# Optimization experiments

Hardware: AMD Instinct MI355X
Metric: run time of the kernel (lower is better)

Reference implementation:

```python
import jax, jax.numpy as jnp
import numpy as np

REG = 1e-6

def maxpool2(x):  # NCHW, kernel 2 stride 2
    return jax.lax.reduce_window(x, -jnp.inf, jax.lax.max, (1, 1, 2, 2), (1, 1, 2, 2), 'VALID')

def conv2d_same(x, w, b):  # NCHW / OIHW, stride 1, padding 1 (3x3)
    y = jax.lax.conv_general_dilated(x, w, (1, 1), ((1, 1), (1, 1)),
                                     dimension_numbers=('NCHW', 'OIHW', 'NCHW'))
    return y + b[None, :, None, None]

def batch_skew(a):  # [B,3] -> [B,3,3]
    z = jnp.zeros_like(a[:, 0])
    return jnp.stack([
        jnp.stack([z, -a[:, 2], a[:, 1]], -1),
        jnp.stack([a[:, 2], z, -a[:, 0]], -1),
        jnp.stack([-a[:, 1], a[:, 0], z], -1)], 1)

def batch_twist2mat(w):  # Rodrigues: so(3) -> SO(3)
    theta = jnp.maximum(jnp.linalg.norm(w, axis=1, keepdims=True), 1e-12)  # [B,1]
    A = batch_skew(w / theta)
    s = jnp.sin(theta)[:, :, None]
    c = (1.0 - jnp.cos(theta))[:, :, None]
    return jnp.eye(3, dtype=w.dtype) + s * A + c * (A @ A)

def setup_inputs() -> dict:
    key = jax.random.key(0)
    ks = jax.random.split(key, 24)
    B, C, H, W = 64, 8, 240, 320
    HW = H * W
    A = jax.random.normal(ks[0], (B, 6, 6), jnp.float32)
    JtJ = A @ jnp.swapaxes(A, 1, 2) + 6.0 * jnp.eye(6, dtype=jnp.float32)  # SPD Hessian
    inp = {
        'JtJ': JtJ,
        'Jt': jax.random.normal(ks[1], (B, 6, HW), jnp.float32),
        'weights': jax.random.uniform(ks[2], (B, 1, H, W), jnp.float32),
        'R': jax.random.normal(ks[3], (B, 1, H, W), jnp.float32),
        'pose_R': jax.random.normal(ks[4], (B, 3, 3), jnp.float32),
        'pose_t': jax.random.normal(ks[5], (B, 3, 1), jnp.float32),
        'invD0': jax.random.uniform(ks[6], (B, 1, H, W), jnp.float32),
        'invD1': jax.random.uniform(ks[7], (B, 1, H, W), jnp.float32),
        'x0': jax.random.normal(ks[8], (B, C, H, W), jnp.float32),
        'x1': jax.random.normal(ks[9], (B, C, H, W), jnp.float32),
        'K': jax.random.normal(ks[10], (B, 3, 3), jnp.float32),
        # DampingNet parameters
        'consts': jax.random.normal(ks[11], (6, 6), jnp.float32),
        'conv1_w': jax.random.normal(ks[12], (8, 1, 3, 3), jnp.float32) * 0.2,
        'conv1_b': jnp.zeros((8,), jnp.float32),
        'conv2_w': jax.random.normal(ks[13], (16, 8, 3, 3), jnp.float32) * 0.1,
        'conv2_b': jnp.zeros((16,), jnp.float32),
        'fc1_w': jax.random.normal(ks[14], (64, 19200), jnp.float32) * 0.01,
        'fc1_b': jnp.zeros((64,), jnp.float32),
        'fc2_w': jax.random.normal(ks[15], (6, 64), jnp.float32) * 0.1,
        'fc2_b': jnp.zeros((6,), jnp.float32),
    }
    return inp

def dampingnet(R, consts, c1w, c1b, c2w, c2b, f1w, f1b, f2w, f2b):
    B = R.shape[0]
    h = maxpool2(R)
    h = jax.nn.relu(conv2d_same(h, c1w, c1b))
    h = maxpool2(h)
    h = jax.nn.relu(conv2d_same(h, c2w, c2b))
    h = maxpool2(h)
    h = h.reshape(B, -1)  # [B, 19200], NCHW flatten matches torch
    h = jax.nn.relu(h @ f1w.T + f1b)
    lambdas_w = jax.nn.softmax(h @ f2w.T + f2b, axis=-1)  # [B,6]
    wc = lambdas_w @ consts  # [B,6]
    min_, max_ = -6.0, -5.0
    return 10.0 ** (min_ + jax.nn.sigmoid(wc) * (max_ - min_))  # [B,6]

def reference(JtJ, Jt, weights, R, pose_R, pose_t, invD0, invD1, x0, x1, K,
              consts, conv1_w, conv1_b, conv2_w, conv2_b, fc1_w, fc1_b, fc2_w, fc2_b):
    B = JtJ.shape[0]
    wR = (weights * R).reshape(B, -1, 1)            # [B,HW,1]
    JtR = Jt @ wR                                   # [B,6,1]
    lam = dampingnet(R, consts, conv1_w, conv1_b, conv2_w, conv2_b,
                     fc1_w, fc1_b, fc2_w, fc2_b)    # [B,6]
    trace = jnp.trace(JtJ, axis1=1, axis2=2)        # [B]
    diag_add = lam + 1e-6 * trace[:, None]          # [B,6]
    eye6 = jnp.eye(6, dtype=JtJ.dtype)
    Hessian = JtJ + diag_add[:, :, None] * eye6     # diag_mask*lambda + epsilon
    # inverse_update_pose: regularized batched 6x6 inverse
    Hinv = jnp.linalg.inv(Hessian + REG * eye6)
    xi = Hinv @ JtR                                 # [B,6,1]
    d_R = batch_twist2mat(-xi[:, :3, 0])            # [B,3,3]
    d_t = -(d_R @ xi[:, 3:])                        # [B,3,1]
    R_new = pose_R @ d_R
    t_new = pose_R @ d_t + pose_t
    return jnp.concatenate([R_new, t_new], axis=2)  # [B,3,4] pose (R|t)
```

## Files before the change

kernel.cpp:

```cpp
#include <hip/hip_runtime.h>
#include <math.h>

#define BATCH 64
#define WW 320
#define HWTOT 76800
#define HW4 19200
#define NJTRB 512
#define JSL4 2400
#define NCONV1 1280
#define KS 96
#define NSLICE 200

__global__ __launch_bounds__(256) void k_front(
    const float* __restrict__ Jt, const float* __restrict__ wgt,
    const float* __restrict__ Rin, const float* __restrict__ c1w,
    const float* __restrict__ c1b, float* __restrict__ part,
    float* __restrict__ h1) {
  __shared__ float smem[34 * 37 + 96];
  int tid = threadIdx.x;
  if (blockIdx.x < NJTRB) {
    int b = blockIdx.x >> 3, s = blockIdx.x & 7;
    const float4* w4 = (const float4*)(wgt + (size_t)b * HWTOT);
    const float4* r4 = (const float4*)(Rin + (size_t)b * HWTOT);
    const float4* j4 = (const float4*)(Jt + (size_t)b * 6 * HWTOT);
    int base = s * JSL4;
    float acc[6] = {0.f, 0.f, 0.f, 0.f, 0.f, 0.f};
#pragma unroll 3
    for (int k = 0; k < 9; ++k) {
      int t = base + k * 256 + tid;
      float4 wv = w4[t], rv = r4[t];
      float4 p;
      p.x = wv.x * rv.x; p.y = wv.y * rv.y; p.z = wv.z * rv.z; p.w = wv.w * rv.w;
#pragma unroll
      for (int i = 0; i < 6; ++i) {
        float4 jv = j4[i * HW4 + t];
        acc[i] += jv.x * p.x + jv.y * p.y + jv.z * p.z + jv.w * p.w;
      }
    }
    if (tid < 96) {
      int t = base + 2304 + tid;
      float4 wv = w4[t], rv = r4[t];
      float4 p;
      p.x = wv.x * rv.x; p.y = wv.y * rv.y; p.z = wv.z * rv.z; p.w = wv.w * rv.w;
#pragma unroll
      for (int i = 0; i < 6; ++i) {
        float4 jv = j4[i * HW4 + t];
        acc[i] += jv.x * p.x + jv.y * p.y + jv.z * p.z + jv.w * p.w;
      }
    }
#pragma unroll
    for (int i = 0; i < 6; ++i) {
      float v = acc[i];
      for (int off = 32; off; off >>= 1) v += __shfl_down(v, off, 64);
      acc[i] = v;
    }
    float* sred = smem;
    int lane = tid & 63, wid = tid >> 6;
    if (lane == 0) {
#pragma unroll
      for (int i = 0; i < 6; ++i) sred[wid * 6 + i] = acc[i];
    }
    __syncthreads();
    if (tid < 6) {
      part[blockIdx.x * 6 + tid] =
          sred[0 + tid] + sred[6 + tid] + sred[12 + tid] + sred[18 + tid];
    }
    return;
  }
  int cb = blockIdx.x - NJTRB;
  int b = cb / 20, rem = cb % 20;
  int by = rem / 5, bx = rem % 5;
  float (*sA)[37] = (float(*)[37])smem;
  float* sW = smem + 34 * 37;
  float* sB = sW + 72;
  if (tid < 72) sW[tid] = c1w[(tid & 7) * 9 + (tid >> 3)];
  if (tid < 8) sB[tid] = c1b[tid];
  int iy0 = 32 * by - 1;
  const float* src = Rin + (size_t)b * HWTOT;
  for (int idx = tid; idx < 34 * 18; idx += 256) {
    int pr = idx / 18, c4 = idx % 18;
    int py = iy0 + pr;
    int gx = 64 * bx - 4 + 4 * c4;
    float cell0 = 0.f, cell1 = 0.f;
    if (py >= 0 && py < 120 && gx >= 0 && gx < 320) {
      const float4* row0 = (const float4*)(src + (size_t)(2 * py) * WW + gx);
      const float4* row1 = (const float4*)(src + (size_t)(2 * py + 1) * WW + gx);
      float4 v0 = row0[0], v1 = row1[0];
      cell0 = fmaxf(fmaxf(v0.x, v0.y), fmaxf(v1.x, v1.y));
      cell1 = fmaxf(fmaxf(v0.z, v0.w), fmaxf(v1.z, v1.w));
    }
    sA[pr][2 * c4] = cell0;
    sA[pr][2 * c4 + 1] = cell1;
  }
  __syncthreads();
  int ly = tid / 16, lx = tid % 16;
  int y = 16 * by + ly, x = 16 * bx + lx;
  float win[16];
#pragma unroll
  for (int r = 0; r < 4; ++r)
#pragma unroll
    for (int c = 0; c < 4; ++c) win[r * 4 + c] = sA[2 * ly + r][2 * lx + c + 1];
  float acc[8][4];
#pragma unroll
  for (int oc = 0; oc < 8; ++oc)
#pragma unroll
    for (int p = 0; p < 4; ++p) acc[oc][p] = 0.f;
#pragma unroll
  for (int tap = 0; tap < 9; ++tap) {
    int ky = tap / 3, kx = tap % 3;
#pragma unroll
    for (int oc = 0; oc < 8; ++oc) {
      float wv = sW[tap * 8 + oc];
#pragma unroll
      for (int py = 0; py < 2; ++py)
#pragma unroll
        for (int px = 0; px < 2; ++px)
          acc[oc][py * 2 + px] += wv * win[(py + ky) * 4 + (px + kx)];
    }
  }
  if (y < 60) {
    float v[8];
#pragma unroll
    for (int oc = 0; oc < 8; ++oc)
      v[oc] = fmaxf(fmaxf(fmaxf(acc[oc][0], acc[oc][1]), fmaxf(acc[oc][2], acc[oc][3])) + sB[oc], 0.f);
    float4* dst = (float4*)(h1 + (((size_t)b * 60 + y) * 80 + x) * 8);
    dst[0] = make_float4(v[0], v[1], v[2], v[3]);
    dst[1] = make_float4(v[4], v[5], v[6], v[7]);
  }
}

__global__ __launch_bounds__(256) void k_conv2(
    const float* __restrict__ h1, const float* __restrict__ c2w,
    const float* __restrict__ c2b, float* __restrict__ h2) {
  __shared__ float sA[8][34][37];
  __shared__ __align__(16) float sW[576];
  __shared__ float sB[8];
  int b = blockIdx.z >> 1, ocg = blockIdx.z & 1;
  int ty0 = blockIdx.y * 16, tx0 = blockIdx.x * 16;
  int tid = threadIdx.x;
  for (int i = tid; i < 576; i += 256) {
    int ic = i / 72, tap = (i % 72) / 8, o = i % 8;
    sW[i] = c2w[(ocg * 8 + o) * 72 + ic * 9 + tap];
  }
  if (tid < 8) sB[tid] = c2b[ocg * 8 + tid];
  int iy0 = ty0 * 2 - 1, ix0 = tx0 * 2 - 1;
  const float* src = h1 + (size_t)b * 60 * 80 * 8;
  for (int idx = tid; idx < 34 * 34; idx += 256) {
    int r = idx / 34, c = idx % 34;
    int gy = iy0 + r, gx = ix0 + c;
    float4 v0 = make_float4(0.f, 0.f, 0.f, 0.f), v1 = v0;
    if (gy >= 0 && gy < 60 && gx >= 0 && gx < 80) {
      const float4* p = (const float4*)(src + ((size_t)gy * 80 + gx) * 8);
      v0 = p[0]; v1 = p[1];
    }
    sA[0][r][c] = v0.x; sA[1][r][c] = v0.y; sA[2][r][c] = v0.z; sA[3][r][c] = v0.w;
    sA[4][r][c] = v1.x; sA[5][r][c] = v1.y; sA[6][r][c] = v1.z; sA[7][r][c] = v1.w;
  }
  __syncthreads();
  int ly = tid / 16, lx = tid % 16;
  int y = ty0 + ly, x = tx0 + lx;
  float acc[8][4];
#pragma unroll
  for (int oc = 0; oc < 8; ++oc)
#pragma unroll
    for (int p = 0; p < 4; ++p) acc[oc][p] = 0.f;
  const float4* sW4 = (const float4*)sW;
#pragma unroll 1
  for (int ic = 0; ic < 8; ++ic) {
    float win[16];
#pragma unroll
    for (int r = 0; r < 4; ++r)
#pragma unroll
      for (int c = 0; c < 4; ++c) win[r * 4 + c] = sA[ic][2 * ly + r][2 * lx + c];
#pragma unroll
    for (int tap = 0; tap < 9; ++tap) {
      int ky = tap / 3, kx = tap % 3;
#pragma unroll
      for (int q = 0; q < 2; ++q) {
        float4 w4v = sW4[(ic * 9 + tap) * 2 + q];
        float warr[4] = {w4v.x, w4v.y, w4v.z, w4v.w};
#pragma unroll
        for (int c4 = 0; c4 < 4; ++c4) {
          float wv = warr[c4];
          int oc = q * 4 + c4;
#pragma unroll
          for (int py = 0; py < 2; ++py)
#pragma unroll
            for (int px = 0; px < 2; ++px)
              acc[oc][py * 2 + px] += wv * win[(py + ky) * 4 + (px + kx)];
        }
      }
    }
  }
  if (y < 30 && x < 40) {
#pragma unroll
    for (int o = 0; o < 8; ++o) {
      int oc = ocg * 8 + o;
      float m = fmaxf(fmaxf(acc[o][0], acc[o][1]), fmaxf(acc[o][2], acc[o][3])) + sB[o];
      h2[(((size_t)b * 16 + oc) * 30 + y) * 40 + x] = fmaxf(m, 0.f);
    }
  }
}

__global__ __launch_bounds__(256) void k_fc1_part(
    const float* __restrict__ h2, const float* __restrict__ f1w,
    float* __restrict__ fcpart) {
  __shared__ __align__(16) float sH[KS * 68];
  __shared__ __align__(16) float sWt[KS * 68];
  int sl = blockIdx.x, k0 = sl * KS;
  int tid = threadIdx.x;
  for (int idx = tid; idx < 64 * KS; idx += 256) {
    int b = idx / KS, kk = idx % KS;
    sH[kk * 68 + b] = h2[(size_t)b * 19200 + k0 + kk];
    sWt[kk * 68 + b] = f1w[(size_t)b * 19200 + k0 + kk];
  }
  __syncthreads();
  int bq = tid & 15, jq = tid >> 4;
  int b0 = bq * 4, j0 = jq * 4;
  float acc[4][4];
#pragma unroll
  for (int i = 0; i < 4; ++i)
#pragma unroll
    for (int j = 0; j < 4; ++j) acc[i][j] = 0.f;
  for (int kk = 0; kk < KS; ++kk) {
    float4 hv = *(const float4*)&sH[kk * 68 + b0];
    float4 wv = *(const float4*)&sWt[kk * 68 + j0];
    float hb[4] = {hv.x, hv.y, hv.z, hv.w};
    float wb[4] = {wv.x, wv.y, wv.z, wv.w};
#pragma unroll
    for (int i = 0; i < 4; ++i)
#pragma unroll
      for (int j = 0; j < 4; ++j) acc[i][j] += hb[i] * wb[j];
  }
#pragma unroll
  for (int i = 0; i < 4; ++i)
#pragma unroll
    for (int j = 0; j < 4; ++j)
      fcpart[(size_t)sl * 4096 + (b0 + i) * 64 + (j0 + j)] = acc[i][j];
}

__global__ __launch_bounds__(256) void k_final(
    const float* __restrict__ fcpart, const float* __restrict__ f1b,
    const float* __restrict__ f2w, const float* __restrict__ f2b,
    const float* __restrict__ consts, const float* __restrict__ part,
    const float* __restrict__ JtJ, const float* __restrict__ poseR,
    const float* __restrict__ poseT, float* __restrict__ out) {
  __shared__ float sfc[4][64];
  __shared__ float fc1v[64];
  __shared__ float lg[6];
  __shared__ float lamv[6];
  __shared__ float jtrv[6];
  int b = blockIdx.x, tid = threadIdx.x;
  int g = tid >> 6, j = tid & 63;
  float a = 0.f;
  for (int s = g; s < NSLICE; s += 4) a += fcpart[(size_t)s * 4096 + b * 64 + j];
  sfc[g][j] = a;
  __syncthreads();
  if (tid < 64)
    fc1v[tid] = fmaxf(sfc[0][tid] + sfc[1][tid] + sfc[2][tid] + sfc[3][tid] + f1b[tid], 0.f);
  if (tid >= 64 && tid < 70) {
    int i = tid - 64;
    float v = 0.f;
    for (int s = 0; s < 8; ++s) v += part[(b * 8 + s) * 6 + i];
    jtrv[i] = v;
  }
  __syncthreads();
  if (tid < 6) {
    float v = f2b[tid];
#pragma unroll
    for (int k = 0; k < 64; ++k) v += fc1v[k] * f2w[tid * 64 + k];
    lg[tid] = v;
  }
  __syncthreads();
  if (tid < 6) {
    float m = lg[0];
#pragma unroll
    for (int i = 1; i < 6; ++i) m = fmaxf(m, lg[i]);
    float e[6], ssum = 0.f;
#pragma unroll
    for (int i = 0; i < 6; ++i) { e[i] = expf(lg[i] - m); ssum += e[i]; }
    float inv = 1.f / ssum;
    float wc = 0.f;
#pragma unroll
    for (int i = 0; i < 6; ++i) wc += (e[i] * inv) * consts[i * 6 + tid];
    float sg = 1.f / (1.f + expf(-wc));
    lamv[tid] = expf((-6.f + sg) * 2.302585092994046f);
  }
  __syncthreads();
  if (tid == 0) {
    float Hm[6][6];
    const float* srcH = JtJ + b * 36;
    float tr = 0.f;
#pragma unroll
    for (int i = 0; i < 6; ++i) {
#pragma unroll
      for (int jj = 0; jj < 6; ++jj) Hm[i][jj] = srcH[i * 6 + jj];
      tr += srcH[i * 6 + i];
    }
    float rhs[6];
#pragma unroll
    for (int i = 0; i < 6; ++i) {
      rhs[i] = jtrv[i];
      Hm[i][i] += lamv[i] + 1e-6f * tr + 1e-6f;
    }
    float L[6][6];
#pragma unroll
    for (int i = 0; i < 6; ++i) {
#pragma unroll
      for (int jj = 0; jj < 6; ++jj) {
        if (jj > i) continue;
        float s = Hm[i][jj];
#pragma unroll
        for (int k = 0; k < 6; ++k)
          if (k < jj) s -= L[i][k] * L[jj][k];
        if (i == jj) L[i][jj] = sqrtf(fmaxf(s, 1e-30f));
        else L[i][jj] = s / L[jj][jj];
      }
    }
    float yv[6];
#pragma unroll
    for (int i = 0; i < 6; ++i) {
      float s = rhs[i];
#pragma unroll
      for (int k = 0; k < 6; ++k)
        if (k < i) s -= L[i][k] * yv[k];
      yv[i] = s / L[i][i];
    }
    float xi[6];
#pragma unroll
    for (int ii = 5; ii >= 0; --ii) {
      float s = yv[ii];
#pragma unroll
      for (int k = 0; k < 6; ++k)
        if (k > ii) s -= L[k][ii] * xi[k];
      xi[ii] = s / L[ii][ii];
    }
    float wx = -xi[0], wy = -xi[1], wz = -xi[2];
    float th = fmaxf(sqrtf(wx * wx + wy * wy + wz * wz), 1e-12f);
    float ux = wx / th, uy = wy / th, uz = wz / th;
    float s = sinf(th), c1 = 1.f - cosf(th);
    float Rd[3][3];
    Rd[0][0] = 1.f + c1 * (ux * ux - 1.f);
    Rd[0][1] = -s * uz + c1 * (ux * uy);
    Rd[0][2] = s * uy + c1 * (ux * uz);
    Rd[1][0] = s * uz + c1 * (uy * ux);
    Rd[1][1] = 1.f + c1 * (uy * uy - 1.f);
    Rd[1][2] = -s * ux + c1 * (uy * uz);
    Rd[2][0] = -s * uy + c1 * (uz * ux);
    Rd[2][1] = s * ux + c1 * (uz * uy);
    Rd[2][2] = 1.f + c1 * (uz * uz - 1.f);
    float dt[3];
#pragma unroll
    for (int r = 0; r < 3; ++r)
      dt[r] = -(Rd[r][0] * xi[3] + Rd[r][1] * xi[4] + Rd[r][2] * xi[5]);
    const float* pR = poseR + b * 9;
    const float* pt = poseT + b * 3;
#pragma unroll
    for (int r = 0; r < 3; ++r) {
#pragma unroll
      for (int cc = 0; cc < 3; ++cc) {
        out[b * 12 + r * 4 + cc] =
            pR[r * 3 + 0] * Rd[0][cc] + pR[r * 3 + 1] * Rd[1][cc] + pR[r * 3 + 2] * Rd[2][cc];
      }
      out[b * 12 + r * 4 + 3] =
          pR[r * 3 + 0] * dt[0] + pR[r * 3 + 1] * dt[1] + pR[r * 3 + 2] * dt[2] + pt[r];
    }
  }
}

extern "C" void kernel_launch(void* const* d_in, const int* in_sizes, int n_in,
                              void* d_out, int out_size, void* d_ws, size_t ws_size,
                              hipStream_t stream) {
  const float* JtJ = (const float*)d_in[0];
  const float* Jt = (const float*)d_in[1];
  const float* wts = (const float*)d_in[2];
  const float* Rin = (const float*)d_in[3];
  const float* poseR = (const float*)d_in[4];
  const float* poseT = (const float*)d_in[5];
  const float* consts = (const float*)d_in[11];
  const float* c1w = (const float*)d_in[12];
  const float* c1b = (const float*)d_in[13];
  const float* c2w = (const float*)d_in[14];
  const float* c2b = (const float*)d_in[15];
  const float* f1w = (const float*)d_in[16];
  const float* f1b = (const float*)d_in[17];
  const float* f2w = (const float*)d_in[18];
  const float* f2b = (const float*)d_in[19];
  float* ws = (float*)d_ws;
  float* part = ws;
  float* h1 = part + 3072;
  float* h2 = h1 + 2457600;
  float* fcpart = h2 + 1228800;
  float* out = (float*)d_out;

  k_front<<<dim3(NJTRB + NCONV1), dim3(256), 0, stream>>>(Jt, wts, Rin, c1w, c1b, part, h1);
  k_conv2<<<dim3(3, 2, BATCH * 2), dim3(256), 0, stream>>>(h1, c2w, c2b, h2);
  k_fc1_part<<<dim3(NSLICE), dim3(256), 0, stream>>>(h2, f1w, fcpart);
  k_final<<<dim3(64), dim3(256), 0, stream>>>(fcpart, f1b, f2w, f2b, consts, part,
                                              JtJ, poseR, poseT, out);
}
```

Before: 77.04 us.

## Spread JtR reduction across all three stage kernels to fill idle CUs

The bandwidth-heavy Jt·(w·R) reduction is split into 16 slices per batch. Twelve slices still run in the front kernel, while two each now run inside the conv2 and fc1 kernels, so those small-grid launches also stream Jt and fill otherwise idle compute units. The conv2 kernel also stages its input channels in two halves, halving its shared memory, and is flattened to a 1D grid. The costs are more partial sums to reduce in the final kernel, extra barriers in conv2, and a risk of lengthening the later stages if they were not actually underutilizing the GPU.

```diff
diff --git a/kernel.cpp b/kernel.cpp
--- a/kernel.cpp
+++ b/kernel.cpp
@@ -5,11 +5,61 @@
 #define WW 320
 #define HWTOT 76800
 #define HW4 19200
-#define NJTRB 512
-#define JSL4 2400
+#define NJTR1 768
+#define NJTR2 128
+#define NJTR3 128
+#define SL4 1200
 #define NCONV1 1280
 #define KS 96
 #define NSLICE 200
+
+__device__ __forceinline__ void jtr_block(
+    const float* __restrict__ Jt, const float* __restrict__ wgt,
+    const float* __restrict__ Rin, float* __restrict__ part,
+    int b, int sg, int base, float* sred) {
+  int tid = threadIdx.x;
+  const float4* w4 = (const float4*)(wgt + (size_t)b * HWTOT);
+  const float4* r4 = (const float4*)(Rin + (size_t)b * HWTOT);
+  const float4* j4 = (const float4*)(Jt + (size_t)b * 6 * HWTOT);
+  float acc[6] = {0.f, 0.f, 0.f, 0.f, 0.f, 0.f};
+#pragma unroll 2
+  for (int k = 0; k < 4; ++k) {
+    int t = base + k * 256 + tid;
+    float4 wv = w4[t], rv = r4[t];
+    float4 p;
+    p.x = wv.x * rv.x; p.y = wv.y * rv.y; p.z = wv.z * rv.z; p.w = wv.w * rv.w;
+#pragma unroll
+    for (int i = 0; i < 6; ++i) {
+      float4 jv = j4[i * HW4 + t];
+      acc[i] += jv.x * p.x + jv.y * p.y + jv.z * p.z + jv.w * p.w;
+    }
+  }
+  if (tid < 176) {
+    int t = base + 1024 + tid;
+    float4 wv = w4[t], rv = r4[t];
+    float4 p;
+    p.x = wv.x * rv.x; p.y = wv.y * rv.y; p.z = wv.z * rv.z; p.w = wv.w * rv.w;
+#pragma unroll
+    for (int i = 0; i < 6; ++i) {
+      float4 jv = j4[i * HW4 + t];
+      acc[i] += jv.x * p.x + jv.y * p.y + jv.z * p.z + jv.w * p.w;
+    }
+  }
+#pragma unroll
+  for (int i = 0; i < 6; ++i) {
+    float v = acc[i];
+    for (int off = 32; off; off >>= 1) v += __shfl_down(v, off, 64);
+    acc[i] = v;
+  }
+  int lane = tid & 63, wid = tid >> 6;
+  if (lane == 0) {
+#pragma unroll
+    for (int i = 0; i < 6; ++i) sred[wid * 6 + i] = acc[i];
+  }
+  __syncthreads();
+  if (tid < 6)
+    part[sg * 6 + tid] = sred[tid] + sred[6 + tid] + sred[12 + tid] + sred[18 + tid];
+}
 
 __global__ __launch_bounds__(256) void k_front(
     const float* __restrict__ Jt, const float* __restrict__ wgt,
@@ -18,56 +68,12 @@
     float* __restrict__ h1) {
   __shared__ float smem[34 * 37 + 96];
   int tid = threadIdx.x;
-  if (blockIdx.x < NJTRB) {
-    int b = blockIdx.x >> 3, s = blockIdx.x & 7;
-    const float4* w4 = (const float4*)(wgt + (size_t)b * HWTOT);
-    const float4* r4 = (const float4*)(Rin + (size_t)b * HWTOT);
-    const float4* j4 = (const float4*)(Jt + (size_t)b * 6 * HWTOT);
-    int base = s * JSL4;
-    float acc[6] = {0.f, 0.f, 0.f, 0.f, 0.f, 0.f};
-#pragma unroll 3
-    for (int k = 0; k < 9; ++k) {
-      int t = base + k * 256 + tid;
-      float4 wv = w4[t], rv = r4[t];
-      float4 p;
-      p.x = wv.x * rv.x; p.y = wv.y * rv.y; p.z = wv.z * rv.z; p.w = wv.w * rv.w;
-#pragma unroll
-      for (int i = 0; i < 6; ++i) {
-        float4 jv = j4[i * HW4 + t];
-        acc[i] += jv.x * p.x + jv.y * p.y + jv.z * p.z + jv.w * p.w;
-      }
-    }
-    if (tid < 96) {
-      int t = base + 2304 + tid;
-      float4 wv = w4[t], rv = r4[t];
-      float4 p;
-      p.x = wv.x * rv.x; p.y = wv.y * rv.y; p.z = wv.z * rv.z; p.w = wv.w * rv.w;
-#pragma unroll
-      for (int i = 0; i < 6; ++i) {
-        float4 jv = j4[i * HW4 + t];
-        acc[i] += jv.x * p.x + jv.y * p.y + jv.z * p.z + jv.w * p.w;
-      }
-    }
-#pragma unroll
-    for (int i = 0; i < 6; ++i) {
-      float v = acc[i];
-      for (int off = 32; off; off >>= 1) v += __shfl_down(v, off, 64);
-      acc[i] = v;
-    }
-    float* sred = smem;
-    int lane = tid & 63, wid = tid >> 6;
-    if (lane == 0) {
-#pragma unroll
-      for (int i = 0; i < 6; ++i) sred[wid * 6 + i] = acc[i];
-    }
-    __syncthreads();
-    if (tid < 6) {
-      part[blockIdx.x * 6 + tid] =
-          sred[0 + tid] + sred[6 + tid] + sred[12 + tid] + sred[18 + tid];
-    }
+  if (blockIdx.x < NJTR1) {
+    int b = blockIdx.x / 12, s = blockIdx.x % 12;
+    jtr_block(Jt, wgt, Rin, part, b, b * 16 + s, s * SL4, smem);
     return;
   }
-  int cb = blockIdx.x - NJTRB;
+  int cb = blockIdx.x - NJTR1;
   int b = cb / 20, rem = cb % 20;
   int by = rem / 5, bx = rem % 5;
   float (*sA)[37] = (float(*)[37])smem;
@@ -129,15 +135,25 @@
   }
 }
 
-__global__ __launch_bounds__(256) void k_conv2(
+__global__ __launch_bounds__(256) void k_mid(
     const float* __restrict__ h1, const float* __restrict__ c2w,
-    const float* __restrict__ c2b, float* __restrict__ h2) {
-  __shared__ float sA[8][34][37];
+    const float* __restrict__ c2b, float* __restrict__ h2,
+    const float* __restrict__ Jt, const float* __restrict__ wgt,
+    const float* __restrict__ Rin, float* __restrict__ part) {
+  __shared__ float sA4[4][34][37];
   __shared__ __align__(16) float sW[576];
   __shared__ float sB[8];
-  int b = blockIdx.z >> 1, ocg = blockIdx.z & 1;
-  int ty0 = blockIdx.y * 16, tx0 = blockIdx.x * 16;
+  __shared__ float sred[24];
   int tid = threadIdx.x;
+  if (blockIdx.x < NJTR2) {
+    int b = blockIdx.x >> 1, s = 12 + (blockIdx.x & 1);
+    jtr_block(Jt, wgt, Rin, part, b, b * 16 + s, s * SL4, sred);
+    return;
+  }
+  int cb = blockIdx.x - NJTR2;
+  int b = cb / 12, rem = cb % 12;
+  int gx = rem % 3, gy = (rem / 3) % 2, ocg = rem / 6;
+  int ty0 = gy * 16, tx0 = gx * 16;
   for (int i = tid; i < 576; i += 256) {
     int ic = i / 72, tap = (i % 72) / 8, o = i % 8;
     sW[i] = c2w[(ocg * 8 + o) * 72 + ic * 9 + tap];
@@ -145,20 +161,7 @@
   if (tid < 8) sB[tid] = c2b[ocg * 8 + tid];
   int iy0 = ty0 * 2 - 1, ix0 = tx0 * 2 - 1;
   const float* src = h1 + (size_t)b * 60 * 80 * 8;
-  for (int idx = tid; idx < 34 * 34; idx += 256) {
-    int r = idx / 34, c = idx % 34;
-    int gy = iy0 + r, gx = ix0 + c;
-    float4 v0 = make_float4(0.f, 0.f, 0.f, 0.f), v1 = v0;
-    if (gy >= 0 && gy < 60 && gx >= 0 && gx < 80) {
-      const float4* p = (const float4*)(src + ((size_t)gy * 80 + gx) * 8);
-      v0 = p[0]; v1 = p[1];
-    }
-    sA[0][r][c] = v0.x; sA[1][r][c] = v0.y; sA[2][r][c] = v0.z; sA[3][r][c] = v0.w;
-    sA[4][r][c] = v1.x; sA[5][r][c] = v1.y; sA[6][r][c] = v1.z; sA[7][r][c] = v1.w;
-  }
-  __syncthreads();
   int ly = tid / 16, lx = tid % 16;
-  int y = ty0 + ly, x = tx0 + lx;
   float acc[8][4];
 #pragma unroll
   for (int oc = 0; oc < 8; ++oc)
@@ -166,32 +169,47 @@
     for (int p = 0; p < 4; ++p) acc[oc][p] = 0.f;
   const float4* sW4 = (const float4*)sW;
 #pragma unroll 1
-  for (int ic = 0; ic < 8; ++ic) {
-    float win[16];
-#pragma unroll
-    for (int r = 0; r < 4; ++r)
-#pragma unroll
-      for (int c = 0; c < 4; ++c) win[r * 4 + c] = sA[ic][2 * ly + r][2 * lx + c];
-#pragma unroll
-    for (int tap = 0; tap < 9; ++tap) {
-      int ky = tap / 3, kx = tap % 3;
-#pragma unroll
-      for (int q = 0; q < 2; ++q) {
-        float4 w4v = sW4[(ic * 9 + tap) * 2 + q];
-        float warr[4] = {w4v.x, w4v.y, w4v.z, w4v.w};
-#pragma unroll
-        for (int c4 = 0; c4 < 4; ++c4) {
-          float wv = warr[c4];
-          int oc = q * 4 + c4;
-#pragma unroll
-          for (int py = 0; py < 2; ++py)
-#pragma unroll
-            for (int px = 0; px < 2; ++px)
-              acc[oc][py * 2 + px] += wv * win[(py + ky) * 4 + (px + kx)];
+  for (int half = 0; half < 2; ++half) {
+    __syncthreads();
+    for (int idx = tid; idx < 34 * 34; idx += 256) {
+      int r = idx / 34, c = idx % 34;
+      int gyy = iy0 + r, gxx = ix0 + c;
+      float4 v = make_float4(0.f, 0.f, 0.f, 0.f);
+      if (gyy >= 0 && gyy < 60 && gxx >= 0 && gxx < 80)
+        v = ((const float4*)(src + ((size_t)gyy * 80 + gxx) * 8))[half];
+      sA4[0][r][c] = v.x; sA4[1][r][c] = v.y; sA4[2][r][c] = v.z; sA4[3][r][c] = v.w;
+    }
+    __syncthreads();
+#pragma unroll 1
+    for (int ic4 = 0; ic4 < 4; ++ic4) {
+      int ic = half * 4 + ic4;
+      float win[16];
+#pragma unroll
+      for (int r = 0; r < 4; ++r)
+#pragma unroll
+        for (int c = 0; c < 4; ++c) win[r * 4 + c] = sA4[ic4][2 * ly + r][2 * lx + c];
+#pragma unroll
+      for (int tap = 0; tap < 9; ++tap) {
+        int ky = tap / 3, kx = tap % 3;
+#pragma unroll
+        for (int q = 0; q < 2; ++q) {
+          float4 w4v = sW4[(ic * 9 + tap) * 2 + q];
+          float warr[4] = {w4v.x, w4v.y, w4v.z, w4v.w};
+#pragma unroll
+          for (int c4 = 0; c4 < 4; ++c4) {
+            float wv = warr[c4];
+            int oc = q * 4 + c4;
+#pragma unroll
+            for (int py = 0; py < 2; ++py)
+#pragma unroll
+              for (int px = 0; px < 2; ++px)
+                acc[oc][py * 2 + px] += wv * win[(py + ky) * 4 + (px + kx)];
+          }
         }
       }
     }
   }
+  int y = ty0 + ly, x = tx0 + lx;
   if (y < 30 && x < 40) {
 #pragma unroll
     for (int o = 0; o < 8; ++o) {
@@ -202,13 +220,20 @@
   }
 }
 
-__global__ __launch_bounds__(256) void k_fc1_part(
+__global__ __launch_bounds__(256) void k_back(
     const float* __restrict__ h2, const float* __restrict__ f1w,
-    float* __restrict__ fcpart) {
+    float* __restrict__ fcpart, const float* __restrict__ Jt,
+    const float* __restrict__ wgt, const float* __restrict__ Rin,
+    float* __restrict__ part) {
   __shared__ __align__(16) float sH[KS * 68];
   __shared__ __align__(16) float sWt[KS * 68];
-  int sl = blockIdx.x, k0 = sl * KS;
   int tid = threadIdx.x;
+  if (blockIdx.x < NJTR3) {
+    int b = blockIdx.x >> 1, s = 14 + (blockIdx.x & 1);
+    jtr_block(Jt, wgt, Rin, part, b, b * 16 + s, s * SL4, sH);
+    return;
+  }
+  int sl = blockIdx.x - NJTR3, k0 = sl * KS;
   for (int idx = tid; idx < 64 * KS; idx += 256) {
     int b = idx / KS, kk = idx % KS;
     sH[kk * 68 + b] = h2[(size_t)b * 19200 + k0 + kk];
@@ -261,7 +286,7 @@
   if (tid >= 64 && tid < 70) {
     int i = tid - 64;
     float v = 0.f;
-    for (int s = 0; s < 8; ++s) v += part[(b * 8 + s) * 6 + i];
+    for (int s = 0; s < 16; ++s) v += part[(b * 16 + s) * 6 + i];
     jtrv[i] = v;
   }
   __syncthreads();
@@ -388,14 +413,14 @@
   const float* f2b = (const float*)d_in[19];
   float* ws = (float*)d_ws;
   float* part = ws;
-  float* h1 = part + 3072;
+  float* h1 = part + 6144;
   float* h2 = h1 + 2457600;
   float* fcpart = h2 + 1228800;
   float* out = (float*)d_out;
 
-  k_front<<<dim3(NJTRB + NCONV1), dim3(256), 0, stream>>>(Jt, wts, Rin, c1w, c1b, part, h1);
-  k_conv2<<<dim3(3, 2, BATCH * 2), dim3(256), 0, stream>>>(h1, c2w, c2b, h2);
-  k_fc1_part<<<dim3(NSLICE), dim3(256), 0, stream>>>(h2, f1w, fcpart);
+  k_front<<<dim3(NJTR1 + NCONV1), dim3(256), 0, stream>>>(Jt, wts, Rin, c1w, c1b, part, h1);
+  k_mid<<<dim3(NJTR2 + 768), dim3(256), 0, stream>>>(h1, c2w, c2b, h2, Jt, wts, Rin, part);
+  k_back<<<dim3(NJTR3 + NSLICE), dim3(256), 0, stream>>>(h2, f1w, fcpart, Jt, wts, Rin, part);
   k_final<<<dim3(64), dim3(256), 0, stream>>>(fcpart, f1b, f2w, f2b, consts, part,
                                               JtJ, poseR, poseT, out);
 }
```

Result: slower. 79.67 us (+3.4%).

## Retile fc1 split-K, transpose partial layout, read conv2 weights directly

Applied to the files above, without the earlier changes.

The fc1 split-K slice shrinks from 96 to 64 so there are 300 slices instead of 200. The partial sums are now stored per batch contiguously, which lets the final kernel reduce them with float4 loads across 16 groups and stage the fc2 weights and consts in shared memory. conv2 no longer stages weights and bias in LDS and reads them directly as uniform global loads with a fully unrolled ic loop. The LDS row pitch also changes to 38. This adds more partial-sum traffic and risks higher register pressure in conv2.

```diff
diff --git a/kernel.cpp b/kernel.cpp
--- a/kernel.cpp
+++ b/kernel.cpp
@@ -8,8 +8,8 @@
 #define NJTRB 512
 #define JSL4 2400
 #define NCONV1 1280
-#define KS 96
-#define NSLICE 200
+#define KS 64
+#define NSLICE 300
 
 __global__ __launch_bounds__(256) void k_front(
     const float* __restrict__ Jt, const float* __restrict__ wgt,
@@ -132,17 +132,10 @@
 __global__ __launch_bounds__(256) void k_conv2(
     const float* __restrict__ h1, const float* __restrict__ c2w,
     const float* __restrict__ c2b, float* __restrict__ h2) {
-  __shared__ float sA[8][34][37];
-  __shared__ __align__(16) float sW[576];
-  __shared__ float sB[8];
+  __shared__ float sA[8][34][38];
   int b = blockIdx.z >> 1, ocg = blockIdx.z & 1;
   int ty0 = blockIdx.y * 16, tx0 = blockIdx.x * 16;
   int tid = threadIdx.x;
-  for (int i = tid; i < 576; i += 256) {
-    int ic = i / 72, tap = (i % 72) / 8, o = i % 8;
-    sW[i] = c2w[(ocg * 8 + o) * 72 + ic * 9 + tap];
-  }
-  if (tid < 8) sB[tid] = c2b[ocg * 8 + tid];
   int iy0 = ty0 * 2 - 1, ix0 = tx0 * 2 - 1;
   const float* src = h1 + (size_t)b * 60 * 80 * 8;
   for (int idx = tid; idx < 34 * 34; idx += 256) {
@@ -158,14 +151,13 @@
   }
   __syncthreads();
   int ly = tid / 16, lx = tid % 16;
-  int y = ty0 + ly, x = tx0 + lx;
   float acc[8][4];
 #pragma unroll
-  for (int oc = 0; oc < 8; ++oc)
-#pragma unroll
-    for (int p = 0; p < 4; ++p) acc[oc][p] = 0.f;
-  const float4* sW4 = (const float4*)sW;
-#pragma unroll 1
+  for (int o = 0; o < 8; ++o)
+#pragma unroll
+    for (int p = 0; p < 4; ++p) acc[o][p] = 0.f;
+  const float* wbase = c2w + ocg * 8 * 72;
+#pragma unroll
   for (int ic = 0; ic < 8; ++ic) {
     float win[16];
 #pragma unroll
@@ -176,27 +168,22 @@
     for (int tap = 0; tap < 9; ++tap) {
       int ky = tap / 3, kx = tap % 3;
 #pragma unroll
-      for (int q = 0; q < 2; ++q) {
-        float4 w4v = sW4[(ic * 9 + tap) * 2 + q];
-        float warr[4] = {w4v.x, w4v.y, w4v.z, w4v.w};
-#pragma unroll
-        for (int c4 = 0; c4 < 4; ++c4) {
-          float wv = warr[c4];
-          int oc = q * 4 + c4;
-#pragma unroll
-          for (int py = 0; py < 2; ++py)
-#pragma unroll
-            for (int px = 0; px < 2; ++px)
-              acc[oc][py * 2 + px] += wv * win[(py + ky) * 4 + (px + kx)];
-        }
+      for (int o = 0; o < 8; ++o) {
+        float wv = wbase[o * 72 + ic * 9 + tap];
+#pragma unroll
+        for (int py = 0; py < 2; ++py)
+#pragma unroll
+          for (int px = 0; px < 2; ++px)
+            acc[o][py * 2 + px] += wv * win[(py + ky) * 4 + (px + kx)];
       }
     }
   }
+  int y = ty0 + ly, x = tx0 + lx;
   if (y < 30 && x < 40) {
 #pragma unroll
     for (int o = 0; o < 8; ++o) {
       int oc = ocg * 8 + o;
-      float m = fmaxf(fmaxf(acc[o][0], acc[o][1]), fmaxf(acc[o][2], acc[o][3])) + sB[o];
+      float m = fmaxf(fmaxf(acc[o][0], acc[o][1]), fmaxf(acc[o][2], acc[o][3])) + c2b[oc];
       h2[(((size_t)b * 16 + oc) * 30 + y) * 40 + x] = fmaxf(m, 0.f);
     }
   }
@@ -210,7 +197,7 @@
   int sl = blockIdx.x, k0 = sl * KS;
   int tid = threadIdx.x;
   for (int idx = tid; idx < 64 * KS; idx += 256) {
-    int b = idx / KS, kk = idx % KS;
+    int b = idx >> 6, kk = idx & 63;
     sH[kk * 68 + b] = h2[(size_t)b * 19200 + k0 + kk];
     sWt[kk * 68 + b] = f1w[(size_t)b * 19200 + k0 + kk];
   }
@@ -236,7 +223,7 @@
   for (int i = 0; i < 4; ++i)
 #pragma unroll
     for (int j = 0; j < 4; ++j)
-      fcpart[(size_t)sl * 4096 + (b0 + i) * 64 + (j0 + j)] = acc[i][j];
+      fcpart[(size_t)(b0 + i) * 19200 + sl * 64 + (j0 + j)] = acc[i][j];
 }
 
 __global__ __launch_bounds__(256) void k_final(
@@ -245,19 +232,28 @@
     const float* __restrict__ consts, const float* __restrict__ part,
     const float* __restrict__ JtJ, const float* __restrict__ poseR,
     const float* __restrict__ poseT, float* __restrict__ out) {
-  __shared__ float sfc[4][64];
+  __shared__ __align__(16) float sred[16 * 64];
   __shared__ float fc1v[64];
+  __shared__ float sf2w[384];
+  __shared__ float sf2b[8];
+  __shared__ float sconst[36];
   __shared__ float lg[6];
   __shared__ float lamv[6];
   __shared__ float jtrv[6];
   int b = blockIdx.x, tid = threadIdx.x;
-  int g = tid >> 6, j = tid & 63;
-  float a = 0.f;
-  for (int s = g; s < NSLICE; s += 4) a += fcpart[(size_t)s * 4096 + b * 64 + j];
-  sfc[g][j] = a;
-  __syncthreads();
-  if (tid < 64)
-    fc1v[tid] = fmaxf(sfc[0][tid] + sfc[1][tid] + sfc[2][tid] + sfc[3][tid] + f1b[tid], 0.f);
+  for (int i = tid; i < 384; i += 256) sf2w[i] = f2w[i];
+  if (tid < 6) sf2b[tid] = f2b[tid];
+  if (tid < 36) sconst[tid] = consts[tid];
+  {
+    const float4* fp4 = (const float4*)(fcpart + (size_t)b * 19200);
+    int sg = tid >> 4, j4 = tid & 15;
+    float4 a = make_float4(0.f, 0.f, 0.f, 0.f);
+    for (int s = sg; s < NSLICE; s += 16) {
+      float4 v = fp4[s * 16 + j4];
+      a.x += v.x; a.y += v.y; a.z += v.z; a.w += v.w;
+    }
+    ((float4*)sred)[sg * 16 + j4] = a;
+  }
   if (tid >= 64 && tid < 70) {
     int i = tid - 64;
     float v = 0.f;
@@ -265,10 +261,17 @@
     jtrv[i] = v;
   }
   __syncthreads();
+  if (tid < 64) {
+    float v = 0.f;
+#pragma unroll
+    for (int sg = 0; sg < 16; ++sg) v += sred[sg * 64 + tid];
+    fc1v[tid] = fmaxf(v + f1b[tid], 0.f);
+  }
+  __syncthreads();
   if (tid < 6) {
-    float v = f2b[tid];
-#pragma unroll
-    for (int k = 0; k < 64; ++k) v += fc1v[k] * f2w[tid * 64 + k];
+    float v = sf2b[tid];
+#pragma unroll
+    for (int k = 0; k < 64; ++k) v += fc1v[k] * sf2w[tid * 64 + k];
     lg[tid] = v;
   }
   __syncthreads();
@@ -282,7 +285,7 @@
     float inv = 1.f / ssum;
     float wc = 0.f;
 #pragma unroll
-    for (int i = 0; i < 6; ++i) wc += (e[i] * inv) * consts[i * 6 + tid];
+    for (int i = 0; i < 6; ++i) wc += (e[i] * inv) * sconst[i * 6 + tid];
     float sg = 1.f / (1.f + expf(-wc));
     lamv[tid] = expf((-6.f + sg) * 2.302585092994046f);
   }
```

Measured after the change: 72.10 us. 6.4% less time.
